# Optimization experiments

Measured on AMD Instinct MI355X. Metric: run time of the kernel, lower is better.

Reference implementation:

```python
import jax, jax.numpy as jnp
import numpy as np

P_TH, N_TH, K, NEGPOS = 0.35, 0.4, 10, 7
V0, V1 = 0.1, 0.2


def point_form(b):
    return jnp.concatenate([b[..., :2] - b[..., 2:] / 2, b[..., :2] + b[..., 2:] / 2], -1)


def decode(loc, priors):
    # standard SSD decode, returns cxcywh (point_form is applied by caller)
    cxcy = priors[..., :2] + loc[..., :2] * V0 * priors[..., 2:]
    wh = priors[..., 2:] * jnp.exp(loc[..., 2:] * V1)
    return jnp.concatenate([cxcy, wh], -1)


def jaccard(a, b):
    # a: [N,4], b: [M,4] corner form -> [N,M] IoU
    tl = jnp.maximum(a[:, None, :2], b[None, :, :2])
    br = jnp.minimum(a[:, None, 2:], b[None, :, 2:])
    wh = jnp.clip(br - tl, 0.0)
    inter = wh[..., 0] * wh[..., 1]
    aa = ((a[:, 2] - a[:, 0]) * (a[:, 3] - a[:, 1]))[:, None]
    ab = ((b[:, 2] - b[:, 0]) * (b[:, 3] - b[:, 1]))[None, :]
    return inter / (aa + ab - inter)


def encode(matched, priors):
    g_cxcy = ((matched[..., :2] + matched[..., 2:]) / 2 - priors[..., :2]) / (V0 * priors[..., 2:])
    g_wh = jnp.log((matched[..., 2:] - matched[..., :2]) / priors[..., 2:]) / V1
    return jnp.concatenate([g_cxcy, g_wh], -1)


def encode_landm(matched, priors):
    m = matched.reshape(matched.shape[:-1] + (5, 2))
    g = (m - priors[..., None, :2]) / (V0 * priors[..., None, 2:])
    return g.reshape(matched.shape[:-1] + (10,))


def match_one(truths, loc_single, priors):
    # sequential per-object topk selection with column invalidation (as in original match())
    A = priors.shape[0]
    O = truths.shape[0]
    dec_pf = point_form(decode(jax.lax.stop_gradient(loc_single), priors))
    iou_a = jaccard(truths, point_form(priors))  # [O, A]
    iou_p = jaccard(truths, dec_pf)              # [O, A]

    def step(carry, i):
        iou_a, iou_p = carry
        va, ia = jax.lax.top_k(iou_a[i], K)
        av = va > P_TH
        av = jnp.where(av.any(), av, jnp.arange(K) == 0)  # fallback: best anchor
        ma = jnp.zeros(A, jnp.int32).at[ia].add(av.astype(jnp.int32)) > 0
        iou_a = jnp.where(ma[None, :], -1.0, iou_a)
        iou_p = jnp.where(ma[None, :], -1.0, iou_p)
        vp, ip = jax.lax.top_k(iou_p[i], K)
        pv = vp > P_TH + 0.05
        mp = jnp.zeros(A, jnp.int32).at[ip].add(pv.astype(jnp.int32)) > 0
        iou_a = jnp.where(mp[None, :], -1.0, iou_a)
        iou_p = jnp.where(mp[None, :], -1.0, iou_p)
        return (iou_a, iou_p), (ia, av, ip, pv)

    (iou_a, iou_p), (ia, av, ip, pv) = jax.lax.scan(step, (iou_a, iou_p), jnp.arange(O))
    p_idx = jnp.concatenate([ia, ip], 1).reshape(-1)    # [O*2K]
    p_valid = jnp.concatenate([av, pv], 1).reshape(-1)  # [O*2K] bool
    maxv = jnp.maximum(iou_a, iou_p).max(0)             # max over cat(IoU_A, IoU_P)
    neg_mask = (maxv != -1.0) & (maxv < N_TH)
    pos_mask = jnp.zeros(A, jnp.int32).at[p_idx].add(p_valid.astype(jnp.int32)) > 0
    conf = jnp.full(A, -2.0)
    conf = jnp.where(pos_mask, 1.0, conf)
    conf = jnp.where(neg_mask, 0.0, conf)
    return p_idx, p_valid, conf


def _smooth_l1(d):
    ad = jnp.abs(d)
    return jnp.where(ad < 1.0, 0.5 * d * d, ad - 0.5)


def reference(loc_data, conf_data, landm_data, priors, targets):
    B, A, _ = loc_data.shape
    O = targets.shape[1]
    truths = targets[..., :4]
    landms = targets[..., 4:14]
    labels = targets[..., 14]

    p_idx, p_valid, conf = jax.vmap(match_one, in_axes=(0, 0, None))(truths, loc_data, priors)
    p_true = jnp.repeat(jnp.arange(O), 2 * K)  # object id per match slot

    gat = jax.vmap(lambda x, i: x[i])
    pri_sel = priors[p_idx]            # [B, P, 4]
    tru_sel = truths[:, p_true, :]     # [B, P, 4]
    landm_sel = landms[:, p_true, :]   # [B, P, 10]
    lab_sel = labels[:, p_true]        # [B, P]

    # localization loss
    loc_p = gat(loc_data, p_idx)                       # [B, P, 4]
    loc_t = encode(tru_sel, pri_sel)
    wf = p_valid.astype(loc_data.dtype)
    loss_l = jnp.sum(_smooth_l1(loc_p - loc_t) * wf[..., None])
    N = jnp.sum(p_valid)

    # landmark loss (only label==1 positives, first 6 landm dims)
    lvalid = p_valid & (lab_sel == 1.0)
    landm_p = gat(landm_data, p_idx)                   # [B, P, 6]
    landm_t = encode_landm(landm_sel, pri_sel)[..., :6]
    loss_landm = jnp.sum(_smooth_l1(landm_p - landm_t) * lvalid.astype(loc_data.dtype)[..., None])
    N1 = jnp.sum(lvalid)

    # classification with hard negative mining
    lse = jax.nn.logsumexp(conf_data, axis=-1)         # [B, A]
    pos = conf == 1.0
    n_pos = pos.sum(1)                                  # [B]
    loss_pos = jnp.sum((lse - conf_data[..., 1]) * pos)
    negc = conf == 0.0
    loss_c = lse - conf_data[..., 0]                    # CE with label 0
    masked = jnp.where(negc, loss_c, -jnp.inf)
    order = jnp.argsort(-masked, axis=1)
    rank = jnp.argsort(order, axis=1)
    neg_sel = (rank < (n_pos * NEGPOS)[:, None]) & negc
    loss_neg = jnp.sum(loss_c * neg_sel)
    loss_cls = loss_pos + loss_neg

    return loss_l / N, loss_cls / N, loss_landm / N1


def setup_inputs() -> dict:
    key = jax.random.key(0)
    ks = jax.random.split(key, 8)
    B, A, O = 16, 65536, 24
    loc_data = jax.random.normal(ks[0], (B, A, 4), jnp.float32) * 0.1
    conf_data = jax.random.normal(ks[1], (B, A, 2), jnp.float32)
    landm_data = jax.random.normal(ks[2], (B, A, 6), jnp.float32)
    # priors: cxcywh in unit square with positive wh
    pc = jax.random.uniform(ks[3], (A, 2), jnp.float32, 0.05, 0.95)
    pwh = jax.random.uniform(ks[4], (A, 2), jnp.float32, 0.02, 0.2)
    priors = jnp.concatenate([pc, pwh], 1)
    # targets: valid corner-form boxes + 10 landm coords + label 1
    tc = jax.random.uniform(ks[5], (B, O, 2), jnp.float32, 0.15, 0.85)
    twh = jax.random.uniform(ks[6], (B, O, 2), jnp.float32, 0.05, 0.25)
    boxes = jnp.concatenate([tc - twh / 2, tc + twh / 2], -1)
    lm = jax.random.uniform(ks[7], (B, O, 10), jnp.float32)
    lab = jnp.ones((B, O, 1), jnp.float32)
    targets = jnp.concatenate([boxes, lm, lab], -1)
    return {"loc_data": loc_data, "conf_data": conf_data, "landm_data": landm_data, "priors": priors, "targets": targets}
```

## Files before the change

### kernel.cpp

```cpp
#include <hip/hip_runtime.h>

#define A_N 65536
#define B_N 16
#define O_N 24
#define KEEP 512
#define CAND_CAP 4096
#define QCAP_W 640
#define PRE_THR 0.1f
#define PF 4

typedef unsigned long long u64;

__device__ __forceinline__ float sl1(float d){
  float ad = fabsf(d);
  return ad < 1.0f ? 0.5f * d * d : ad - 0.5f;
}

__device__ __forceinline__ float iou_parts(float tx1, float ty1, float tx2, float ty2,
                                           float aa, float bx1, float by1, float bx2, float by2){
  float tlx = fmaxf(tx1, bx1), tly = fmaxf(ty1, by1);
  float brx = fminf(tx2, bx2), bry = fminf(ty2, by2);
  float w = fmaxf(brx - tlx, 0.0f), h = fmaxf(bry - tly, 0.0f);
  float inter = w * h;
  float ab = (bx2 - bx1) * (by2 - by1);
  return inter / (aa + ab - inter);
}

__global__ __launch_bounds__(256) void prep_kernel(const float* __restrict__ loc,
    const float* __restrict__ priors, float4* __restrict__ dec,
    float4* __restrict__ pf, unsigned char* __restrict__ flags){
  const int a = blockIdx.x * 256 + threadIdx.x;
  const int b = blockIdx.y;
  const float4 pr = ((const float4*)priors)[a];
  const float4 l = ((const float4*)loc)[(size_t)b * A_N + a];
  float cx = pr.x + l.x * 0.1f * pr.z;
  float cy = pr.y + l.y * 0.1f * pr.w;
  float w  = pr.z * expf(l.z * 0.2f);
  float h  = pr.w * expf(l.w * 0.2f);
  float4 d;
  d.x = cx - w * 0.5f; d.y = cy - h * 0.5f;
  d.z = cx + w * 0.5f; d.w = cy + h * 0.5f;
  dec[(size_t)b * A_N + a] = d;
  if (b == 0){
    float4 p;
    p.x = pr.x - pr.z * 0.5f; p.y = pr.y - pr.w * 0.5f;
    p.z = pr.x + pr.z * 0.5f; p.w = pr.y + pr.w * 0.5f;
    pf[a] = p;
  }
  flags[(size_t)b * A_N + a] = 0;
}

__device__ __forceinline__ void wave_sort_512(u64* sk, int base, int lane, bool asc){
  for (int k = 2; k <= 512; k <<= 1){
    for (int j = k >> 1; j > 0; j >>= 1){
      #pragma unroll
      for (int s = 0; s < 8; ++s){
        int t = lane + s * 64;
        int x = t ^ j;
        if (x > t){
          u64 ka = sk[base + t], kb = sk[base + x];
          bool up = (((t & k) == 0) != asc);
          bool sw = up ? (kb > ka) : (ka > kb);
          if (sw){ sk[base + t] = kb; sk[base + x] = ka; }
        }
      }
      __builtin_amdgcn_wave_barrier();
    }
  }
}

__device__ __forceinline__ void wave_sort_1024(u64* sk, int base, int lane, bool asc){
  for (int k = 2; k <= 1024; k <<= 1){
    for (int j = k >> 1; j > 0; j >>= 1){
      #pragma unroll
      for (int s = 0; s < 16; ++s){
        int t = lane + s * 64;
        int x = t ^ j;
        if (x > t){
          u64 ka = sk[base + t], kb = sk[base + x];
          bool up = (((t & k) == 0) != asc);
          bool sw = up ? (kb > ka) : (ka > kb);
          if (sw){ sk[base + t] = kb; sk[base + x] = ka; }
        }
      }
      __builtin_amdgcn_wave_barrier();
    }
  }
}

__global__ __launch_bounds__(256) void sel_kernel(const float4* __restrict__ dec,
    const float4* __restrict__ pf, const float* __restrict__ targets,
    unsigned char* __restrict__ flags,
    float* __restrict__ out_vals, int* __restrict__ out_idxs){
  __shared__ u64 cand[CAND_CAP];
  __shared__ unsigned qbuf[4][QCAP_W];
  __shared__ unsigned hist[2048];
  __shared__ int s_candCnt, s_b1;
  const int r = blockIdx.x;
  const int type = r & 1;
  const int o = (r >> 1) % O_N;
  const int b = r / (O_N * 2);
  const int tid = threadIdx.x;
  const int w = tid >> 6;
  const int lane = tid & 63;
  const u64 lmask = (1ull << lane) - 1ull;
  const float* tg = targets + (size_t)(b * O_N + o) * 15;
  const float tx1 = tg[0], ty1 = tg[1], tx2 = tg[2], ty2 = tg[3];
  const float aa = (tx2 - tx1) * (ty2 - ty1);
  const float4* src = (type == 0) ? pf : (dec + (size_t)b * A_N);
  unsigned char* fl = flags + (size_t)b * A_N;
  unsigned* myq = qbuf[w];

  if (tid == 0) s_candCnt = 0;
  __syncthreads();

  int qcnt = 0;
  const int abase = w * (A_N / 4);
  const int NCH = (A_N / 4) / 64;
  float4 nxt[PF];
  #pragma unroll
  for (int u = 0; u < PF; ++u) nxt[u] = src[abase + u * 64 + lane];
  for (int c = 0; c < NCH; c += PF){
    float4 cur[PF];
    #pragma unroll
    for (int u = 0; u < PF; ++u) cur[u] = nxt[u];
    if (c + PF < NCH){
      #pragma unroll
      for (int u = 0; u < PF; ++u) nxt[u] = src[abase + (c + PF + u) * 64 + lane];
    }
    #pragma unroll
    for (int u = 0; u < PF; ++u){
      const int a = abase + (c + u) * 64 + lane;
      const float4 bb = cur[u];
      bool ov = (fminf(tx2, bb.z) > fmaxf(tx1, bb.x)) && (fminf(ty2, bb.w) > fmaxf(ty1, bb.y));
      u64 m = __ballot(ov);
      if (ov) myq[qcnt + (int)__popcll(m & lmask)] = (unsigned)a;
      qcnt += (int)__popcll(m);
    }
    if (qcnt > QCAP_W - PF * 64){
      int trips = (qcnt + 63) >> 6;
      int a0 = 0; float4 cb;
      if (lane < qcnt){ a0 = (int)myq[lane]; cb = src[a0]; }
      for (int tr = 0; tr < trips; ++tr){
        int i = tr * 64 + lane;
        bool valid = i < qcnt;
        int a1 = 0; float4 nb;
        int i2 = i + 64;
        if (i2 < qcnt){ a1 = (int)myq[i2]; nb = src[a1]; }
        float v = valid ? iou_parts(tx1, ty1, tx2, ty2, aa, cb.x, cb.y, cb.z, cb.w) : 0.0f;
        if (valid && v >= 0.4f) fl[a0] = 1;
        bool acc = valid && (v > PRE_THR);
        u64 m = __ballot(acc);
        if (m){
          int base = 0;
          if (lane == 0) base = atomicAdd(&s_candCnt, (int)__popcll(m));
          base = __shfl(base, 0);
          if (acc){
            int p = base + (int)__popcll(m & lmask);
            if (p < CAND_CAP) cand[p] = ((u64)__float_as_uint(v) << 32) | (u64)(~(unsigned)a0);
          }
        }
        a0 = a1; cb = nb;
      }
      qcnt = 0;
    }
  }
  {
    int trips = (qcnt + 63) >> 6;
    int a0 = 0; float4 cb;
    if (lane < qcnt){ a0 = (int)myq[lane]; cb = src[a0]; }
    for (int tr = 0; tr < trips; ++tr){
      int i = tr * 64 + lane;
      bool valid = i < qcnt;
      int a1 = 0; float4 nb;
      int i2 = i + 64;
      if (i2 < qcnt){ a1 = (int)myq[i2]; nb = src[a1]; }
      float v = valid ? iou_parts(tx1, ty1, tx2, ty2, aa, cb.x, cb.y, cb.z, cb.w) : 0.0f;
      if (valid && v >= 0.4f) fl[a0] = 1;
      bool acc = valid && (v > PRE_THR);
      u64 m = __ballot(acc);
      if (m){
        int base = 0;
        if (lane == 0) base = atomicAdd(&s_candCnt, (int)__popcll(m));
        base = __shfl(base, 0);
        if (acc){
          int p = base + (int)__popcll(m & lmask);
          if (p < CAND_CAP) cand[p] = ((u64)__float_as_uint(v) << 32) | (u64)(~(unsigned)a0);
        }
      }
      a0 = a1; cb = nb;
    }
  }
  __syncthreads();
  int tot = s_candCnt;
  if (tot < KEEP || tot > CAND_CAP){
    for (int j = tid; j < 2048; j += 256) hist[j] = 0u;
    if (tid == 0) s_candCnt = 0;
    __syncthreads();
    for (int a = tid; a < A_N; a += 256){
      float4 bb = src[a];
      float v = iou_parts(tx1, ty1, tx2, ty2, aa, bb.x, bb.y, bb.z, bb.w);
      if (v > 0.0f){
        unsigned bin = __float_as_uint(v) >> 19;
        if (bin > 2047u) bin = 2047u;
        atomicAdd(&hist[bin], 1u);
      }
    }
    __syncthreads();
    if (tid == 0){
      int cum = 0, b1 = -1;
      for (int bin = 2047; bin >= 0; --bin){
        cum += (int)hist[bin];
        if (cum >= KEEP){ b1 = bin; break; }
      }
      s_b1 = (b1 < 0) ? 0 : b1;
    }
    __syncthreads();
    const int b1 = s_b1;
    for (int a = tid; a < A_N; a += 256){
      float4 bb = src[a];
      float v = iou_parts(tx1, ty1, tx2, ty2, aa, bb.x, bb.y, bb.z, bb.w);
      unsigned bits = __float_as_uint(v);
      unsigned bin = bits >> 19;
      if (bin > 2047u) bin = 2047u;
      bool acc = (v > 0.0f) && ((int)bin >= b1);
      u64 m = __ballot(acc);
      if (m){
        int base = 0;
        if (lane == 0) base = atomicAdd(&s_candCnt, (int)__popcll(m));
        base = __shfl(base, 0);
        if (acc){
          int p = base + (int)__popcll(m & lmask);
          if (p < CAND_CAP) cand[p] = ((u64)bits << 32) | (u64)(~(unsigned)a);
        }
      }
    }
    __syncthreads();
    tot = s_candCnt;
    if (tot > CAND_CAP) tot = CAND_CAP;
  }
  if (tot <= 2048){
    for (int j = tot + tid; j < 2048; j += 256) cand[j] = 0ull;
    __syncthreads();
    wave_sort_512(cand, w * 512, lane, (w & 1) != 0);
    __syncthreads();
    for (int k = 1024; k <= 2048; k <<= 1){
      for (int j = k >> 1; j > 0; j >>= 1){
        for (int t = tid; t < 2048; t += 256){
          int x = t ^ j;
          if (x > t){
            u64 ka = cand[t], kb = cand[x];
            bool up = ((t & k) == 0);
            bool sw = up ? (kb > ka) : (ka > kb);
            if (sw){ cand[t] = kb; cand[x] = ka; }
          }
        }
        __syncthreads();
      }
    }
  } else {
    for (int j = tot + tid; j < CAND_CAP; j += 256) cand[j] = 0ull;
    __syncthreads();
    wave_sort_1024(cand, w * 1024, lane, (w & 1) != 0);
    __syncthreads();
    for (int k = 2048; k <= 4096; k <<= 1){
      for (int j = k >> 1; j > 0; j >>= 1){
        for (int t = tid; t < 4096; t += 256){
          int x = t ^ j;
          if (x > t){
            u64 ka = cand[t], kb = cand[x];
            bool up = ((t & k) == 0);
            bool sw = up ? (kb > ka) : (ka > kb);
            if (sw){ cand[t] = kb; cand[x] = ka; }
          }
        }
        __syncthreads();
      }
    }
  }
  for (int jj = tid; jj < KEEP; jj += 256){
    u64 kk = cand[jj];
    out_vals[(size_t)r * KEEP + jj] = __uint_as_float((unsigned)(kk >> 32));
    out_idxs[(size_t)r * KEEP + jj] = (kk == 0ull) ? 0 : (int)(~(unsigned)kk);
  }
}

__global__ __launch_bounds__(64) void scan_kernel(const float* __restrict__ vals,
    const int* __restrict__ idxs, int* __restrict__ p_idx, int* __restrict__ p_valid,
    unsigned int* __restrict__ bitset_g, int* __restrict__ n_pos_g){
  __shared__ unsigned int bs[A_N / 32];
  __shared__ float pv0[48][64];
  __shared__ int pi0[48][64];
  __shared__ float s_v[10];
  __shared__ int s_i[10];
  const int b = blockIdx.x;
  const int lane = threadIdx.x;
  for (int j = lane; j < A_N / 32; j += 64) bs[j] = 0u;
  for (int row = 0; row < 48; ++row){
    pv0[row][lane] = vals[(size_t)(b * 48 + row) * KEEP + lane];
    pi0[row][lane] = idxs[(size_t)(b * 48 + row) * KEEP + lane];
  }
  __syncthreads();
  int npos = 0;
  const float PTH2 = (float)(0.35 + 0.05);
  for (int o = 0; o < O_N; ++o){
    for (int ph = 0; ph < 2; ++ph){
      const int row48 = o * 2 + ph;
      const int r = b * 48 + row48;
      const float* rv = vals + (size_t)r * KEEP;
      const int* ri = idxs + (size_t)r * KEEP;
      int found = 0;
      for (int pos = 0; pos < KEEP && found < 10; pos += 64){
        float v; int id;
        if (pos == 0){ v = pv0[row48][lane]; id = pi0[row48][lane]; }
        else { v = rv[pos + lane]; id = ri[pos + lane]; }
        bool unm = ((bs[id >> 5] >> (id & 31)) & 1u) == 0u;
        unsigned long long m = __ballot(unm);
        int rank = found + __popcll(m & ((1ull << lane) - 1ull));
        if (unm && rank < 10){ s_v[rank] = v; s_i[rank] = id; }
        int add = __popcll(m);
        found = (found + add > 10) ? 10 : (found + add);
        __syncthreads();
      }
      if (lane == 0){
        const float th = (ph == 0) ? 0.35f : PTH2;
        float fv[10]; int fi[10]; int vv[10];
        bool any = false;
        for (int j = 0; j < 10; ++j){
          fv[j] = (j < found) ? s_v[j] : 0.0f;
          fi[j] = (j < found) ? s_i[j] : 0;
          vv[j] = (fv[j] > th) ? 1 : 0;
          any = any || (vv[j] != 0);
        }
        if (ph == 0 && !any) vv[0] = 1;
        int base_slot = b * (O_N * 20) + o * 20 + ph * 10;
        for (int j = 0; j < 10; ++j){
          p_idx[base_slot + j] = fi[j];
          p_valid[base_slot + j] = vv[j];
          if (vv[j]){
            bs[fi[j] >> 5] |= (1u << (fi[j] & 31));
            npos++;
          }
        }
      }
      __syncthreads();
    }
  }
  for (int j = lane; j < A_N / 32; j += 64) bitset_g[b * (A_N / 32) + j] = bs[j];
  if (lane == 0) n_pos_g[b] = npos;
}

__global__ __launch_bounds__(256) void anchor_kernel(const float* __restrict__ conf,
    const unsigned char* __restrict__ flags, const unsigned int* __restrict__ bitset_g,
    float* __restrict__ lossc, float* __restrict__ partial){
  const int b = blockIdx.y;
  const int a = blockIdx.x * 256 + threadIdx.x;
  __shared__ float red[256];
  bool masked = ((bitset_g[b * (A_N / 32) + (a >> 5)] >> (a & 31)) & 1u) != 0u;
  const float2 c = ((const float2*)conf)[(size_t)b * A_N + a];
  float mx = fmaxf(c.x, c.y);
  float lse = mx + log1pf(expf(-fabsf(c.x - c.y)));
  float lp = 0.0f;
  float lc = -1.0f;
  if (masked) lp = lse - c.y;
  else if (!flags[(size_t)b * A_N + a]) lc = lse - c.x;
  lossc[(size_t)b * A_N + a] = lc;
  red[threadIdx.x] = lp; __syncthreads();
  for (int s = 128; s > 0; s >>= 1){
    if (threadIdx.x < s) red[threadIdx.x] += red[threadIdx.x + s];
    __syncthreads();
  }
  if (threadIdx.x == 0) partial[blockIdx.y * gridDim.x + blockIdx.x] = red[0];
}

__global__ __launch_bounds__(1024) void mine_kernel(const float* __restrict__ lossc,
    const int* __restrict__ n_pos_g, double* __restrict__ accum){
  __shared__ unsigned hist[8192];
  __shared__ u64 sk[2048];
  __shared__ unsigned gsum_s[256];
  __shared__ int s_b1, s_need, s_cnt;
  __shared__ float red[1024];
  const int b = blockIdx.x;
  const int tid = threadIdx.x;
  const int w = tid >> 6;
  const int lane = tid & 63;
  const u64 lmask = (1ull << lane) - 1ull;
  const float4* lc4 = (const float4*)(lossc + (size_t)b * A_N);
  const int M = n_pos_g[b] * 7;
  if (M <= 0) return;
  for (int j = tid; j < 8192; j += 1024) hist[j] = 0u;
  if (tid == 0) s_cnt = 0;
  __syncthreads();
  for (int q = tid; q < A_N / 4; q += 1024){
    float4 v4 = lc4[q];
    float vv[4] = {v4.x, v4.y, v4.z, v4.w};
    #pragma unroll
    for (int e = 0; e < 4; ++e){
      if (vv[e] >= 0.0f){
        unsigned bin = __float_as_uint(vv[e]) >> 19;
        if (bin > 8191u) bin = 8191u;
        atomicAdd(&hist[bin], 1u);
      }
    }
  }
  __syncthreads();
  if (tid < 256){
    unsigned s = 0;
    #pragma unroll
    for (int e = 0; e < 32; ++e) s += hist[tid * 32 + e];
    gsum_s[tid] = s;
  }
  __syncthreads();
  if (tid == 0){
    int cum = 0, b1 = -1, need = 0;
    for (int g = 255; g >= 0 && b1 < 0; --g){
      unsigned gs = gsum_s[g];
      if (cum + (int)gs >= M){
        for (int bin = g * 32 + 31; bin >= g * 32; --bin){
          int cc = (int)hist[bin];
          if (cum + cc >= M){ b1 = bin; need = M - cum; break; }
          cum += cc;
        }
      } else cum += (int)gs;
    }
    s_b1 = b1;
    s_need = need;
  }
  __syncthreads();
  const int b1 = s_b1;
  const int need = s_need;
  float sum = 0.0f;
  for (int q = tid; q < A_N / 4; q += 1024){
    float4 v4 = lc4[q];
    float vv[4] = {v4.x, v4.y, v4.z, v4.w};
    #pragma unroll
    for (int e = 0; e < 4; ++e){
      float v = vv[e];
      bool isneg = (v >= 0.0f);
      unsigned bits = __float_as_uint(v);
      unsigned bin = bits >> 19;
      if (bin > 8191u) bin = 8191u;
      if (isneg && (int)bin > b1) sum += v;
      bool acc = isneg && ((int)bin == b1);
      u64 m = __ballot(acc);
      if (m){
        int base = 0;
        if (lane == 0) base = atomicAdd(&s_cnt, (int)__popcll(m));
        base = __shfl(base, 0);
        if (acc){
          int p = base + (int)__popcll(m & lmask);
          if (p < 2048) sk[p] = (u64)bits;
        }
      }
    }
  }
  __syncthreads();
  int cnt = s_cnt; if (cnt > 2048) cnt = 2048;
  for (int j = cnt + tid; j < 2048; j += 1024) sk[j] = 0ull;
  __syncthreads();
  if (w < 4) wave_sort_512(sk, w * 512, lane, (w & 1) != 0);
  __syncthreads();
  for (int k = 1024; k <= 2048; k <<= 1){
    for (int j = k >> 1; j > 0; j >>= 1){
      for (int t = tid; t < 2048; t += 1024){
        int x = t ^ j;
        if (x > t){
          u64 ka = sk[t], kb = sk[x];
          bool up = ((t & k) == 0);
          bool sw = up ? (kb > ka) : (ka > kb);
          if (sw){ sk[t] = kb; sk[x] = ka; }
        }
      }
      __syncthreads();
    }
  }
  for (int i = tid; i < need; i += 1024) sum += __uint_as_float((unsigned)sk[i]);
  red[tid] = sum; __syncthreads();
  for (int s = 512; s > 0; s >>= 1){
    if (tid < s) red[tid] += red[tid + s];
    __syncthreads();
  }
  if (tid == 0) atomicAdd(&accum[3], (double)red[0]);
}

__global__ __launch_bounds__(512) void loss_lm_kernel(const float* __restrict__ loc,
    const float* __restrict__ landm, const float* __restrict__ priors,
    const float* __restrict__ targets, const int* __restrict__ p_idx,
    const int* __restrict__ p_valid, double* __restrict__ accum, int* __restrict__ cnts){
  const int b = blockIdx.x;
  const int j = threadIdx.x;
  float ll = 0.0f, lmv = 0.0f;
  int nv = 0, nv1 = 0;
  if (j < 480){
    int valid = p_valid[b * 480 + j];
    if (valid){
      int pid = p_idx[b * 480 + j];
      int t = j / 20;
      const float* tg = targets + (size_t)(b * O_N + t) * 15;
      float4 pr = ((const float4*)priors)[pid];
      float4 lp = ((const float4*)loc)[(size_t)b * A_N + pid];
      float gcx = ((tg[0] + tg[2]) * 0.5f - pr.x) / (0.1f * pr.z);
      float gcy = ((tg[1] + tg[3]) * 0.5f - pr.y) / (0.1f * pr.w);
      float gw = logf((tg[2] - tg[0]) / pr.z) / 0.2f;
      float gh = logf((tg[3] - tg[1]) / pr.w) / 0.2f;
      ll = sl1(lp.x - gcx) + sl1(lp.y - gcy) + sl1(lp.z - gw) + sl1(lp.w - gh);
      nv = 1;
      if (tg[14] == 1.0f){
        nv1 = 1;
        const float* lmp = landm + ((size_t)b * A_N + pid) * 6;
        for (int k = 0; k < 3; ++k){
          float gx = (tg[4 + 2 * k] - pr.x) / (0.1f * pr.z);
          float gy = (tg[5 + 2 * k] - pr.y) / (0.1f * pr.w);
          lmv += sl1(lmp[2 * k] - gx) + sl1(lmp[2 * k + 1] - gy);
        }
      }
    }
  }
  __shared__ float redf[512];
  __shared__ int redi[512];
  redf[j] = ll; __syncthreads();
  for (int s = 256; s > 0; s >>= 1){ if (j < s) redf[j] += redf[j + s]; __syncthreads(); }
  float llT = redf[0]; __syncthreads();
  redf[j] = lmv; __syncthreads();
  for (int s = 256; s > 0; s >>= 1){ if (j < s) redf[j] += redf[j + s]; __syncthreads(); }
  float lmT = redf[0]; __syncthreads();
  redi[j] = nv; __syncthreads();
  for (int s = 256; s > 0; s >>= 1){ if (j < s) redi[j] += redi[j + s]; __syncthreads(); }
  int nT = redi[0]; __syncthreads();
  redi[j] = nv1; __syncthreads();
  for (int s = 256; s > 0; s >>= 1){ if (j < s) redi[j] += redi[j + s]; __syncthreads(); }
  int n1T = redi[0];
  if (j == 0){
    atomicAdd(&accum[0], (double)llT);
    atomicAdd(&accum[1], (double)lmT);
    atomicAdd(&cnts[0], nT);
    atomicAdd(&cnts[1], n1T);
  }
}

__global__ __launch_bounds__(256) void final_kernel(const double* __restrict__ accum,
    const int* __restrict__ cnts, const float* __restrict__ partial, int npart,
    float* __restrict__ out){
  __shared__ double red[256];
  double s = 0.0;
  for (int i = threadIdx.x; i < npart; i += 256) s += (double)partial[i];
  red[threadIdx.x] = s; __syncthreads();
  for (int st = 128; st > 0; st >>= 1){
    if (threadIdx.x < st) red[threadIdx.x] += red[threadIdx.x + st];
    __syncthreads();
  }
  if (threadIdx.x == 0){
    double N = (double)cnts[0];
    double N1 = (double)cnts[1];
    out[0] = (float)(accum[0] / N);
    out[1] = (float)((red[0] + accum[3]) / N);
    out[2] = (float)(accum[1] / N1);
  }
}

extern "C" void kernel_launch(void* const* d_in, const int* in_sizes, int n_in,
                              void* d_out, int out_size, void* d_ws, size_t ws_size,
                              hipStream_t stream){
  (void)in_sizes; (void)n_in; (void)out_size; (void)ws_size;
  const float* loc     = (const float*)d_in[0];
  const float* conf    = (const float*)d_in[1];
  const float* landm   = (const float*)d_in[2];
  const float* priors  = (const float*)d_in[3];
  const float* targets = (const float*)d_in[4];
  float* out = (float*)d_out;
  char* ws = (char*)d_ws;

  double* accum = (double*)ws;
  int* cnts = (int*)(ws + 32);
  size_t off = 64;
  float4* dec = (float4*)(ws + off);  off += (size_t)B_N * A_N * 16;
  float4* pf  = (float4*)(ws + off);  off += (size_t)A_N * 16;
  unsigned char* flags = (unsigned char*)(ws + off); off += (size_t)B_N * A_N;
  float* vals = (float*)(ws + off); off += (size_t)B_N * O_N * 2 * KEEP * 4;
  int* idxs   = (int*)(ws + off);   off += (size_t)B_N * O_N * 2 * KEEP * 4;
  int* p_idx  = (int*)(ws + off);   off += (size_t)B_N * 480 * 4;
  int* p_val  = (int*)(ws + off);   off += (size_t)B_N * 480 * 4;
  unsigned int* bitset = (unsigned int*)(ws + off); off += (size_t)B_N * (A_N / 32) * 4;
  int* n_pos  = (int*)(ws + off);   off += 64;
  float* lossc = (float*)(ws + off); off += (size_t)B_N * A_N * 4;
  float* partial = (float*)(ws + off); off += (size_t)B_N * (A_N / 256) * 4;

  hipMemsetAsync(ws, 0, 64, stream);
  hipLaunchKernelGGL(prep_kernel, dim3(A_N / 256, B_N), dim3(256), 0, stream,
                     loc, priors, dec, pf, flags);
  hipLaunchKernelGGL(sel_kernel, dim3(B_N * O_N * 2), dim3(256), 0, stream,
                     dec, pf, targets, flags, vals, idxs);
  hipLaunchKernelGGL(scan_kernel, dim3(B_N), dim3(64), 0, stream,
                     vals, idxs, p_idx, p_val, bitset, n_pos);
  hipLaunchKernelGGL(anchor_kernel, dim3(A_N / 256, B_N), dim3(256), 0, stream,
                     conf, flags, bitset, lossc, partial);
  hipLaunchKernelGGL(mine_kernel, dim3(B_N), dim3(1024), 0, stream,
                     lossc, n_pos, accum);
  hipLaunchKernelGGL(loss_lm_kernel, dim3(B_N), dim3(512), 0, stream,
                     loc, landm, priors, targets, p_idx, p_val, accum, cnts);
  hipLaunchKernelGGL(final_kernel, dim3(1), dim3(256), 0, stream,
                     accum, cnts, partial, B_N * (A_N / 256), out);
}
```

Before: 463.9 us.

## Precompute per-object overlap lists and fuse anchor loss into mining kernel

Adds a presel kernel that tests each anchor chunk against all 24 targets once and writes compact per-(batch,object,type) index lists. The sel kernel then computes IoU only over those lists, recomputing decoded boxes on the fly, instead of having every block scan all 65536 anchors. The materialised decoded-box buffer is dropped, and the separate anchor_kernel and final partial reduction are folded into mine_kernel, which now has only 16 blocks doing the per-anchor softmax work. The costs are global atomics, an extra launch, and small candidate lists that no longer apply the 0.1 prefilter. Lists larger than 8192 entries fall back to the full scan.

New measurement: 712.1 us. 53.5% more time.

```diff
diff --git a/kernel.cpp b/kernel.cpp
--- a/kernel.cpp
+++ b/kernel.cpp
@@ -4,10 +4,8 @@
 #define B_N 16
 #define O_N 24
 #define KEEP 512
-#define CAND_CAP 4096
-#define QCAP_W 640
-#define PRE_THR 0.1f
-#define PF 4
+#define CAP 8192
+#define CHUNK 2048
 
 typedef unsigned long long u64;
 
@@ -26,13 +24,7 @@
   return inter / (aa + ab - inter);
 }
 
-__global__ __launch_bounds__(256) void prep_kernel(const float* __restrict__ loc,
-    const float* __restrict__ priors, float4* __restrict__ dec,
-    float4* __restrict__ pf, unsigned char* __restrict__ flags){
-  const int a = blockIdx.x * 256 + threadIdx.x;
-  const int b = blockIdx.y;
-  const float4 pr = ((const float4*)priors)[a];
-  const float4 l = ((const float4*)loc)[(size_t)b * A_N + a];
+__device__ __forceinline__ float4 decode_pf(float4 pr, float4 l){
   float cx = pr.x + l.x * 0.1f * pr.z;
   float cy = pr.y + l.y * 0.1f * pr.w;
   float w  = pr.z * expf(l.z * 0.2f);
@@ -40,14 +32,81 @@
   float4 d;
   d.x = cx - w * 0.5f; d.y = cy - h * 0.5f;
   d.z = cx + w * 0.5f; d.w = cy + h * 0.5f;
-  dec[(size_t)b * A_N + a] = d;
-  if (b == 0){
-    float4 p;
-    p.x = pr.x - pr.z * 0.5f; p.y = pr.y - pr.w * 0.5f;
-    p.z = pr.x + pr.z * 0.5f; p.w = pr.y + pr.w * 0.5f;
-    pf[a] = p;
-  }
-  flags[(size_t)b * A_N + a] = 0;
+  return d;
+}
+
+__global__ __launch_bounds__(256) void prep_kernel(const float* __restrict__ priors,
+    float4* __restrict__ pf){
+  const int a = blockIdx.x * 256 + threadIdx.x;
+  const float4 pr = ((const float4*)priors)[a];
+  float4 p;
+  p.x = pr.x - pr.z * 0.5f; p.y = pr.y - pr.w * 0.5f;
+  p.z = pr.x + pr.z * 0.5f; p.w = pr.y + pr.w * 0.5f;
+  pf[a] = p;
+}
+
+__global__ __launch_bounds__(256) void presel_kernel(const float* __restrict__ loc,
+    const float* __restrict__ priors, const float4* __restrict__ pf,
+    const float* __restrict__ targets,
+    unsigned short* __restrict__ glist, int* __restrict__ counts){
+  __shared__ float tbx[O_N * 4];
+  __shared__ unsigned short buf[CHUNK];
+  __shared__ int s_bcnt, s_gbase;
+  const int c = blockIdx.x;
+  const int b = blockIdx.y;
+  const int t = blockIdx.z;
+  const int tid = threadIdx.x;
+  const int lane = tid & 63;
+  const u64 lmask = (1ull << lane) - 1ull;
+  const int base = c * CHUNK;
+  float4 box[8];
+  if (t == 0){
+    #pragma unroll
+    for (int s = 0; s < 8; ++s) box[s] = pf[base + s * 256 + tid];
+  } else {
+    #pragma unroll
+    for (int s = 0; s < 8; ++s){
+      const int a = base + s * 256 + tid;
+      float4 pr = ((const float4*)priors)[a];
+      float4 l = ((const float4*)loc)[(size_t)b * A_N + a];
+      box[s] = decode_pf(pr, l);
+    }
+  }
+  if (tid < O_N * 4) tbx[tid] = targets[(size_t)(b * O_N + (tid >> 2)) * 15 + (tid & 3)];
+  if (tid == 0) s_bcnt = 0;
+  __syncthreads();
+  for (int o = 0; o < O_N; ++o){
+    const float tx1 = tbx[o * 4 + 0], ty1 = tbx[o * 4 + 1];
+    const float tx2 = tbx[o * 4 + 2], ty2 = tbx[o * 4 + 3];
+    #pragma unroll
+    for (int s = 0; s < 8; ++s){
+      const float4 bb = box[s];
+      bool ov = (fminf(tx2, bb.z) > fmaxf(tx1, bb.x)) && (fminf(ty2, bb.w) > fmaxf(ty1, bb.y));
+      u64 m = __ballot(ov);
+      if (m){
+        int wb = 0;
+        if (lane == 0) wb = atomicAdd(&s_bcnt, (int)__popcll(m));
+        wb = __shfl(wb, 0);
+        if (ov) buf[wb + (int)__popcll(m & lmask)] = (unsigned short)(base + s * 256 + tid);
+      }
+    }
+    __syncthreads();
+    const int n = s_bcnt;
+    const int row = (b * O_N + o) * 2 + t;
+    if (n > 0){
+      if (tid == 0) s_gbase = atomicAdd(&counts[row], n);
+      __syncthreads();
+      const int gb = s_gbase;
+      unsigned short* gl = glist + (size_t)row * CAP;
+      for (int j = tid; j < n; j += 256){
+        int p = gb + j;
+        if (p < CAP) gl[p] = buf[j];
+      }
+    }
+    __syncthreads();
+    if (tid == 0) s_bcnt = 0;
+    __syncthreads();
+  }
 }
 
 __device__ __forceinline__ void wave_sort_512(u64* sk, int base, int lane, bool asc){
@@ -88,16 +147,18 @@
   }
 }
 
-__global__ __launch_bounds__(256) void sel_kernel(const float4* __restrict__ dec,
-    const float4* __restrict__ pf, const float* __restrict__ targets,
+__global__ __launch_bounds__(256) void sel_kernel(const float* __restrict__ loc,
+    const float* __restrict__ priors, const float4* __restrict__ pf,
+    const float* __restrict__ targets,
+    const unsigned short* __restrict__ glist, const int* __restrict__ counts,
     unsigned char* __restrict__ flags,
     float* __restrict__ out_vals, int* __restrict__ out_idxs){
-  __shared__ u64 cand[CAND_CAP];
-  __shared__ unsigned qbuf[4][QCAP_W];
+  __shared__ u64 cand[4096];
   __shared__ unsigned hist[2048];
-  __shared__ int s_candCnt, s_b1;
+  __shared__ unsigned gsum_s[64];
+  __shared__ int s_cnt, s_b1;
   const int r = blockIdx.x;
-  const int type = r & 1;
+  const int t = r & 1;
   const int o = (r >> 1) % O_N;
   const int b = r / (O_N * 2);
   const int tid = threadIdx.x;
@@ -107,99 +168,89 @@
   const float* tg = targets + (size_t)(b * O_N + o) * 15;
   const float tx1 = tg[0], ty1 = tg[1], tx2 = tg[2], ty2 = tg[3];
   const float aa = (tx2 - tx1) * (ty2 - ty1);
-  const float4* src = (type == 0) ? pf : (dec + (size_t)b * A_N);
+  const float4* pr4 = (const float4*)priors;
+  const float4* l4 = ((const float4*)loc) + (size_t)b * A_N;
   unsigned char* fl = flags + (size_t)b * A_N;
-  unsigned* myq = qbuf[w];
-
-  if (tid == 0) s_candCnt = 0;
-  __syncthreads();
-
-  int qcnt = 0;
-  const int abase = w * (A_N / 4);
-  const int NCH = (A_N / 4) / 64;
-  float4 nxt[PF];
-  #pragma unroll
-  for (int u = 0; u < PF; ++u) nxt[u] = src[abase + u * 64 + lane];
-  for (int c = 0; c < NCH; c += PF){
-    float4 cur[PF];
-    #pragma unroll
-    for (int u = 0; u < PF; ++u) cur[u] = nxt[u];
-    if (c + PF < NCH){
-      #pragma unroll
-      for (int u = 0; u < PF; ++u) nxt[u] = src[abase + (c + PF + u) * 64 + lane];
-    }
-    #pragma unroll
-    for (int u = 0; u < PF; ++u){
-      const int a = abase + (c + u) * 64 + lane;
-      const float4 bb = cur[u];
-      bool ov = (fminf(tx2, bb.z) > fmaxf(tx1, bb.x)) && (fminf(ty2, bb.w) > fmaxf(ty1, bb.y));
-      u64 m = __ballot(ov);
-      if (ov) myq[qcnt + (int)__popcll(m & lmask)] = (unsigned)a;
-      qcnt += (int)__popcll(m);
-    }
-    if (qcnt > QCAP_W - PF * 64){
-      int trips = (qcnt + 63) >> 6;
-      int a0 = 0; float4 cb;
-      if (lane < qcnt){ a0 = (int)myq[lane]; cb = src[a0]; }
-      for (int tr = 0; tr < trips; ++tr){
-        int i = tr * 64 + lane;
-        bool valid = i < qcnt;
-        int a1 = 0; float4 nb;
-        int i2 = i + 64;
-        if (i2 < qcnt){ a1 = (int)myq[i2]; nb = src[a1]; }
-        float v = valid ? iou_parts(tx1, ty1, tx2, ty2, aa, cb.x, cb.y, cb.z, cb.w) : 0.0f;
-        if (valid && v >= 0.4f) fl[a0] = 1;
-        bool acc = valid && (v > PRE_THR);
+  const unsigned short* gl = glist + (size_t)r * CAP;
+  const int cnt_raw = counts[r];
+  int tot;
+  if (cnt_raw <= CAP){
+    const int cnt = cnt_raw;
+    if (cnt <= 2048){
+      for (int j = tid; j < cnt; j += 256){
+        const int a = gl[j];
+        const float4 bb = (t == 0) ? pf[a] : decode_pf(pr4[a], l4[a]);
+        const float v = iou_parts(tx1, ty1, tx2, ty2, aa, bb.x, bb.y, bb.z, bb.w);
+        if (v >= 0.4f) fl[a] = 1;
+        cand[j] = ((u64)__float_as_uint(v) << 32) | (u64)(~(unsigned)a);
+      }
+      tot = cnt;
+    } else {
+      for (int j = tid; j < 2048; j += 256) hist[j] = 0u;
+      if (tid == 0) s_cnt = 0;
+      __syncthreads();
+      for (int j = tid; j < cnt; j += 256){
+        const int a = gl[j];
+        const float4 bb = (t == 0) ? pf[a] : decode_pf(pr4[a], l4[a]);
+        const float v = iou_parts(tx1, ty1, tx2, ty2, aa, bb.x, bb.y, bb.z, bb.w);
+        if (v >= 0.4f) fl[a] = 1;
+        unsigned bin = __float_as_uint(v) >> 19;
+        if (bin > 2047u) bin = 2047u;
+        atomicAdd(&hist[bin], 1u);
+      }
+      __syncthreads();
+      if (tid < 64){
+        unsigned s = 0;
+        #pragma unroll
+        for (int e = 0; e < 32; ++e) s += hist[tid * 32 + e];
+        gsum_s[tid] = s;
+      }
+      __syncthreads();
+      if (tid == 0){
+        int cum = 0, b1 = -1;
+        for (int g = 63; g >= 0 && b1 < 0; --g){
+          unsigned gs = gsum_s[g];
+          if (cum + (int)gs >= KEEP){
+            for (int bin = g * 32 + 31; bin >= g * 32; --bin){
+              cum += (int)hist[bin];
+              if (cum >= KEEP){ b1 = bin; break; }
+            }
+          } else cum += (int)gs;
+        }
+        s_b1 = (b1 < 0) ? 0 : b1;
+      }
+      __syncthreads();
+      const int b1 = s_b1;
+      for (int j = tid; j < cnt; j += 256){
+        const int a = gl[j];
+        const float4 bb = (t == 0) ? pf[a] : decode_pf(pr4[a], l4[a]);
+        const float v = iou_parts(tx1, ty1, tx2, ty2, aa, bb.x, bb.y, bb.z, bb.w);
+        unsigned bits = __float_as_uint(v);
+        unsigned bin = bits >> 19;
+        if (bin > 2047u) bin = 2047u;
+        bool acc = ((int)bin >= b1);
         u64 m = __ballot(acc);
         if (m){
           int base = 0;
-          if (lane == 0) base = atomicAdd(&s_candCnt, (int)__popcll(m));
+          if (lane == 0) base = atomicAdd(&s_cnt, (int)__popcll(m));
           base = __shfl(base, 0);
           if (acc){
             int p = base + (int)__popcll(m & lmask);
-            if (p < CAND_CAP) cand[p] = ((u64)__float_as_uint(v) << 32) | (u64)(~(unsigned)a0);
+            if (p < 4096) cand[p] = ((u64)bits << 32) | (u64)(~(unsigned)a);
           }
         }
-        a0 = a1; cb = nb;
-      }
-      qcnt = 0;
-    }
-  }
-  {
-    int trips = (qcnt + 63) >> 6;
-    int a0 = 0; float4 cb;
-    if (lane < qcnt){ a0 = (int)myq[lane]; cb = src[a0]; }
-    for (int tr = 0; tr < trips; ++tr){
-      int i = tr * 64 + lane;
-      bool valid = i < qcnt;
-      int a1 = 0; float4 nb;
-      int i2 = i + 64;
-      if (i2 < qcnt){ a1 = (int)myq[i2]; nb = src[a1]; }
-      float v = valid ? iou_parts(tx1, ty1, tx2, ty2, aa, cb.x, cb.y, cb.z, cb.w) : 0.0f;
-      if (valid && v >= 0.4f) fl[a0] = 1;
-      bool acc = valid && (v > PRE_THR);
-      u64 m = __ballot(acc);
-      if (m){
-        int base = 0;
-        if (lane == 0) base = atomicAdd(&s_candCnt, (int)__popcll(m));
-        base = __shfl(base, 0);
-        if (acc){
-          int p = base + (int)__popcll(m & lmask);
-          if (p < CAND_CAP) cand[p] = ((u64)__float_as_uint(v) << 32) | (u64)(~(unsigned)a0);
-        }
-      }
-      a0 = a1; cb = nb;
-    }
-  }
-  __syncthreads();
-  int tot = s_candCnt;
-  if (tot < KEEP || tot > CAND_CAP){
+      }
+      __syncthreads();
+      tot = s_cnt; if (tot > 4096) tot = 4096;
+    }
+  } else {
     for (int j = tid; j < 2048; j += 256) hist[j] = 0u;
-    if (tid == 0) s_candCnt = 0;
+    if (tid == 0) s_cnt = 0;
     __syncthreads();
     for (int a = tid; a < A_N; a += 256){
-      float4 bb = src[a];
-      float v = iou_parts(tx1, ty1, tx2, ty2, aa, bb.x, bb.y, bb.z, bb.w);
+      const float4 bb = (t == 0) ? pf[a] : decode_pf(pr4[a], l4[a]);
+      const float v = iou_parts(tx1, ty1, tx2, ty2, aa, bb.x, bb.y, bb.z, bb.w);
+      if (v >= 0.4f) fl[a] = 1;
       if (v > 0.0f){
         unsigned bin = __float_as_uint(v) >> 19;
         if (bin > 2047u) bin = 2047u;
@@ -207,19 +258,31 @@
       }
     }
     __syncthreads();
+    if (tid < 64){
+      unsigned s = 0;
+      #pragma unroll
+      for (int e = 0; e < 32; ++e) s += hist[tid * 32 + e];
+      gsum_s[tid] = s;
+    }
+    __syncthreads();
     if (tid == 0){
       int cum = 0, b1 = -1;
-      for (int bin = 2047; bin >= 0; --bin){
-        cum += (int)hist[bin];
-        if (cum >= KEEP){ b1 = bin; break; }
+      for (int g = 63; g >= 0 && b1 < 0; --g){
+        unsigned gs = gsum_s[g];
+        if (cum + (int)gs >= KEEP){
+          for (int bin = g * 32 + 31; bin >= g * 32; --bin){
+            cum += (int)hist[bin];
+            if (cum >= KEEP){ b1 = bin; break; }
+          }
+        } else cum += (int)gs;
       }
       s_b1 = (b1 < 0) ? 0 : b1;
     }
     __syncthreads();
     const int b1 = s_b1;
     for (int a = tid; a < A_N; a += 256){
-      float4 bb = src[a];
-      float v = iou_parts(tx1, ty1, tx2, ty2, aa, bb.x, bb.y, bb.z, bb.w);
+      const float4 bb = (t == 0) ? pf[a] : decode_pf(pr4[a], l4[a]);
+      const float v = iou_parts(tx1, ty1, tx2, ty2, aa, bb.x, bb.y, bb.z, bb.w);
       unsigned bits = __float_as_uint(v);
       unsigned bin = bits >> 19;
       if (bin > 2047u) bin = 2047u;
@@ -227,17 +290,16 @@
       u64 m = __ballot(acc);
       if (m){
         int base = 0;
-        if (lane == 0) base = atomicAdd(&s_candCnt, (int)__popcll(m));
+        if (lane == 0) base = atomicAdd(&s_cnt, (int)__popcll(m));
         base = __shfl(base, 0);
         if (acc){
           int p = base + (int)__popcll(m & lmask);
-          if (p < CAND_CAP) cand[p] = ((u64)bits << 32) | (u64)(~(unsigned)a);
-        }
-      }
-    }
-    __syncthreads();
-    tot = s_candCnt;
-    if (tot > CAND_CAP) tot = CAND_CAP;
+          if (p < 4096) cand[p] = ((u64)bits << 32) | (u64)(~(unsigned)a);
+        }
+      }
+    }
+    __syncthreads();
+    tot = s_cnt; if (tot > 4096) tot = 4096;
   }
   if (tot <= 2048){
     for (int j = tot + tid; j < 2048; j += 256) cand[j] = 0ull;
@@ -246,32 +308,32 @@
     __syncthreads();
     for (int k = 1024; k <= 2048; k <<= 1){
       for (int j = k >> 1; j > 0; j >>= 1){
-        for (int t = tid; t < 2048; t += 256){
-          int x = t ^ j;
-          if (x > t){
-            u64 ka = cand[t], kb = cand[x];
-            bool up = ((t & k) == 0);
+        for (int t2 = tid; t2 < 2048; t2 += 256){
+          int x = t2 ^ j;
+          if (x > t2){
+            u64 ka = cand[t2], kb = cand[x];
+            bool up = ((t2 & k) == 0);
             bool sw = up ? (kb > ka) : (ka > kb);
-            if (sw){ cand[t] = kb; cand[x] = ka; }
+            if (sw){ cand[t2] = kb; cand[x] = ka; }
           }
         }
         __syncthreads();
       }
     }
   } else {
-    for (int j = tot + tid; j < CAND_CAP; j += 256) cand[j] = 0ull;
+    for (int j = tot + tid; j < 4096; j += 256) cand[j] = 0ull;
     __syncthreads();
     wave_sort_1024(cand, w * 1024, lane, (w & 1) != 0);
     __syncthreads();
     for (int k = 2048; k <= 4096; k <<= 1){
       for (int j = k >> 1; j > 0; j >>= 1){
-        for (int t = tid; t < 4096; t += 256){
-          int x = t ^ j;
-          if (x > t){
-            u64 ka = cand[t], kb = cand[x];
-            bool up = ((t & k) == 0);
+        for (int t2 = tid; t2 < 4096; t2 += 256){
+          int x = t2 ^ j;
+          if (x > t2){
+            u64 ka = cand[t2], kb = cand[x];
+            bool up = ((t2 & k) == 0);
             bool sw = up ? (kb > ka) : (ka > kb);
-            if (sw){ cand[t] = kb; cand[x] = ka; }
+            if (sw){ cand[t2] = kb; cand[x] = ka; }
           }
         }
         __syncthreads();
@@ -350,31 +412,9 @@
   if (lane == 0) n_pos_g[b] = npos;
 }
 
-__global__ __launch_bounds__(256) void anchor_kernel(const float* __restrict__ conf,
+__global__ __launch_bounds__(1024) void mine_kernel(const float* __restrict__ conf,
     const unsigned char* __restrict__ flags, const unsigned int* __restrict__ bitset_g,
-    float* __restrict__ lossc, float* __restrict__ partial){
-  const int b = blockIdx.y;
-  const int a = blockIdx.x * 256 + threadIdx.x;
-  __shared__ float red[256];
-  bool masked = ((bitset_g[b * (A_N / 32) + (a >> 5)] >> (a & 31)) & 1u) != 0u;
-  const float2 c = ((const float2*)conf)[(size_t)b * A_N + a];
-  float mx = fmaxf(c.x, c.y);
-  float lse = mx + log1pf(expf(-fabsf(c.x - c.y)));
-  float lp = 0.0f;
-  float lc = -1.0f;
-  if (masked) lp = lse - c.y;
-  else if (!flags[(size_t)b * A_N + a]) lc = lse - c.x;
-  lossc[(size_t)b * A_N + a] = lc;
-  red[threadIdx.x] = lp; __syncthreads();
-  for (int s = 128; s > 0; s >>= 1){
-    if (threadIdx.x < s) red[threadIdx.x] += red[threadIdx.x + s];
-    __syncthreads();
-  }
-  if (threadIdx.x == 0) partial[blockIdx.y * gridDim.x + blockIdx.x] = red[0];
-}
-
-__global__ __launch_bounds__(1024) void mine_kernel(const float* __restrict__ lossc,
-    const int* __restrict__ n_pos_g, double* __restrict__ accum){
+    const int* __restrict__ n_pos_g, float* __restrict__ lossc, double* __restrict__ accum){
   __shared__ unsigned hist[8192];
   __shared__ u64 sk[2048];
   __shared__ unsigned gsum_s[256];
@@ -385,25 +425,36 @@
   const int w = tid >> 6;
   const int lane = tid & 63;
   const u64 lmask = (1ull << lane) - 1ull;
-  const float4* lc4 = (const float4*)(lossc + (size_t)b * A_N);
-  const int M = n_pos_g[b] * 7;
-  if (M <= 0) return;
+  const float2* c2 = ((const float2*)conf) + (size_t)b * A_N;
+  const unsigned char* fl = flags + (size_t)b * A_N;
+  const unsigned int* bs = bitset_g + b * (A_N / 32);
+  float* lc = lossc + (size_t)b * A_N;
   for (int j = tid; j < 8192; j += 1024) hist[j] = 0u;
   if (tid == 0) s_cnt = 0;
   __syncthreads();
-  for (int q = tid; q < A_N / 4; q += 1024){
-    float4 v4 = lc4[q];
-    float vv[4] = {v4.x, v4.y, v4.z, v4.w};
-    #pragma unroll
-    for (int e = 0; e < 4; ++e){
-      if (vv[e] >= 0.0f){
-        unsigned bin = __float_as_uint(vv[e]) >> 19;
-        if (bin > 8191u) bin = 8191u;
-        atomicAdd(&hist[bin], 1u);
-      }
-    }
-  }
-  __syncthreads();
+  float lp = 0.0f;
+  for (int a = tid; a < A_N; a += 1024){
+    bool masked = ((bs[a >> 5] >> (a & 31)) & 1u) != 0u;
+    float2 c = c2[a];
+    float mx = fmaxf(c.x, c.y);
+    float lse = mx + log1pf(expf(-fabsf(c.x - c.y)));
+    float v = -1.0f;
+    if (masked) lp += lse - c.y;
+    else if (!fl[a]) v = lse - c.x;
+    lc[a] = v;
+    if (v >= 0.0f){
+      unsigned bin = __float_as_uint(v) >> 19;
+      if (bin > 8191u) bin = 8191u;
+      atomicAdd(&hist[bin], 1u);
+    }
+  }
+  red[tid] = lp; __syncthreads();
+  for (int s = 512; s > 0; s >>= 1){
+    if (tid < s) red[tid] += red[tid + s];
+    __syncthreads();
+  }
+  if (tid == 0) atomicAdd(&accum[2], (double)red[0]);
+  const int M = n_pos_g[b] * 7;
   if (tid < 256){
     unsigned s = 0;
     #pragma unroll
@@ -430,6 +481,7 @@
   const int b1 = s_b1;
   const int need = s_need;
   float sum = 0.0f;
+  const float4* lc4 = (const float4*)lc;
   for (int q = tid; q < A_N / 4; q += 1024){
     float4 v4 = lc4[q];
     float vv[4] = {v4.x, v4.y, v4.z, v4.w};
@@ -538,22 +590,13 @@
   }
 }
 
-__global__ __launch_bounds__(256) void final_kernel(const double* __restrict__ accum,
-    const int* __restrict__ cnts, const float* __restrict__ partial, int npart,
-    float* __restrict__ out){
-  __shared__ double red[256];
-  double s = 0.0;
-  for (int i = threadIdx.x; i < npart; i += 256) s += (double)partial[i];
-  red[threadIdx.x] = s; __syncthreads();
-  for (int st = 128; st > 0; st >>= 1){
-    if (threadIdx.x < st) red[threadIdx.x] += red[threadIdx.x + st];
-    __syncthreads();
-  }
-  if (threadIdx.x == 0){
+__global__ void final_kernel(const double* __restrict__ accum,
+    const int* __restrict__ cnts, float* __restrict__ out){
+  if (threadIdx.x == 0 && blockIdx.x == 0){
     double N = (double)cnts[0];
     double N1 = (double)cnts[1];
     out[0] = (float)(accum[0] / N);
-    out[1] = (float)((red[0] + accum[3]) / N);
+    out[1] = (float)((accum[2] + accum[3]) / N);
     out[2] = (float)(accum[1] / N1);
   }
 }
@@ -572,10 +615,11 @@
 
   double* accum = (double*)ws;
   int* cnts = (int*)(ws + 32);
-  size_t off = 64;
-  float4* dec = (float4*)(ws + off);  off += (size_t)B_N * A_N * 16;
+  int* counts = (int*)(ws + 64);
+  unsigned char* flags = (unsigned char*)(ws + 4096);
+  size_t off = 4096 + (size_t)B_N * A_N;
   float4* pf  = (float4*)(ws + off);  off += (size_t)A_N * 16;
-  unsigned char* flags = (unsigned char*)(ws + off); off += (size_t)B_N * A_N;
+  unsigned short* glist = (unsigned short*)(ws + off); off += (size_t)B_N * O_N * 2 * CAP * 2;
   float* vals = (float*)(ws + off); off += (size_t)B_N * O_N * 2 * KEEP * 4;
   int* idxs   = (int*)(ws + off);   off += (size_t)B_N * O_N * 2 * KEEP * 4;
   int* p_idx  = (int*)(ws + off);   off += (size_t)B_N * 480 * 4;
@@ -583,21 +627,19 @@
   unsigned int* bitset = (unsigned int*)(ws + off); off += (size_t)B_N * (A_N / 32) * 4;
   int* n_pos  = (int*)(ws + off);   off += 64;
   float* lossc = (float*)(ws + off); off += (size_t)B_N * A_N * 4;
-  float* partial = (float*)(ws + off); off += (size_t)B_N * (A_N / 256) * 4;
-
-  hipMemsetAsync(ws, 0, 64, stream);
-  hipLaunchKernelGGL(prep_kernel, dim3(A_N / 256, B_N), dim3(256), 0, stream,
-                     loc, priors, dec, pf, flags);
+
+  hipMemsetAsync(ws, 0, 4096 + (size_t)B_N * A_N, stream);
+  hipLaunchKernelGGL(prep_kernel, dim3(A_N / 256), dim3(256), 0, stream,
+                     priors, pf);
+  hipLaunchKernelGGL(presel_kernel, dim3(A_N / CHUNK, B_N, 2), dim3(256), 0, stream,
+                     loc, priors, pf, targets, glist, counts);
   hipLaunchKernelGGL(sel_kernel, dim3(B_N * O_N * 2), dim3(256), 0, stream,
-                     dec, pf, targets, flags, vals, idxs);
+                     loc, priors, pf, targets, glist, counts, flags, vals, idxs);
   hipLaunchKernelGGL(scan_kernel, dim3(B_N), dim3(64), 0, stream,
                      vals, idxs, p_idx, p_val, bitset, n_pos);
-  hipLaunchKernelGGL(anchor_kernel, dim3(A_N / 256, B_N), dim3(256), 0, stream,
-                     conf, flags, bitset, lossc, partial);
   hipLaunchKernelGGL(mine_kernel, dim3(B_N), dim3(1024), 0, stream,
-                     lossc, n_pos, accum);
+                     conf, flags, bitset, n_pos, lossc, accum);
   hipLaunchKernelGGL(loss_lm_kernel, dim3(B_N), dim3(512), 0, stream,
                      loc, landm, priors, targets, p_idx, p_val, accum, cnts);
-  hipLaunchKernelGGL(final_kernel, dim3(1), dim3(256), 0, stream,
-                     accum, cnts, partial, B_N * (A_N / 256), out);
-}
+  hipLaunchKernelGGL(final_kernel, dim3(1), dim3(64), 0, stream, accum, cnts, out);
+}
```
